# Kernel optimization log

Hardware: AMD Instinct MI355X
Metric: run time of the kernel (lower is better)

The kernel has to match this reference:

```python
import jax, jax.numpy as jnp
import numpy as np

CV_CHAN = 49  # displacement channels; radius = (CV_CHAN - 1) // 2 = 24


def conv1x1(x, W, b):
    # x: [B,C,H,Wd], W: [O,C], b: [O] -> [B,O,H,Wd]
    return jnp.einsum('oc,bchw->bohw', W, x) + b[None, :, None, None]


def corr_volume(f1, f2, radius, eps):
    """Shift-and-dot correlation along width. f1,f2: [B,C,H,W] -> [B,2r+1,H,W].
    Channel k corresponds to displacement d = k - radius; out-of-range positions are 0
    (handled by zero-padding, matching the torch zero-filled shifted tensors)."""
    f1n = f1 / (jnp.linalg.norm(f1, axis=1, keepdims=True) + eps)
    f2n = f2 / (jnp.linalg.norm(f2, axis=1, keepdims=True) + eps)
    Wd = f1.shape[3]
    pad = jnp.pad(f2n, ((0, 0), (0, 0), (0, 0), (radius, radius)))
    # shifted_k[x] = f2n[x - d] = pad[x + 2*radius - k]
    slices = [
        jnp.sum(f1n * jax.lax.dynamic_slice_in_dim(pad, 2 * radius - k, Wd, axis=3), axis=1)
        for k in range(2 * radius + 1)
    ]
    return jnp.stack(slices, axis=1)


def setup_inputs() -> dict:
    key = jax.random.key(0)
    ks = jax.random.split(key, 10)
    B, C, H, W = 4, 128, 128, 256
    F = 128  # fmap channels
    G = 96   # geo encoder output channels
    s = 0.05
    return {
        'feat_l1': jax.random.normal(ks[0], (B, C, H, W), jnp.float32),
        'feat_r1': jax.random.normal(ks[1], (B, C, H, W), jnp.float32),
        'cv0': jax.random.normal(ks[2], (B, CV_CHAN, H, W), jnp.float32),
        'cv1': jax.random.normal(ks[3], (B, CV_CHAN, H, W), jnp.float32),
        'cv2': jax.random.normal(ks[4], (B, CV_CHAN, H, W), jnp.float32),
        'W_f1': jax.random.normal(ks[5], (F, C), jnp.float32) * s,
        'b_f1': jnp.zeros((F,), jnp.float32),
        'W_f2': jax.random.normal(ks[6], (F, C), jnp.float32) * s,
        'b_f2': jnp.zeros((F,), jnp.float32),
        'W_geo': jax.random.normal(ks[7], (G, CV_CHAN), jnp.float32) * s,
        'b_geo': jnp.zeros((G,), jnp.float32),
        'W_sel': jax.random.normal(ks[8], (3, 3 * G), jnp.float32) * s,
        'b_sel': jnp.zeros((3,), jnp.float32),
    }


def reference(feat_l1, feat_r1, cv0, cv1, cv2,
              W_f1, b_f1, W_f2, b_f2, W_geo, b_geo, W_sel, b_sel):
    # init feature maps (init_fmap1 / init_fmap2 as 1x1 convs)
    fmap1 = conv1x1(feat_l1, W_f1, b_f1)
    fmap2 = conv1x1(feat_r1, W_f2, b_f2)
    radius = (CV_CHAN - 1) // 2
    init_corr = corr_volume(fmap1, fmap2, radius, 1e-8)  # [B, CV_CHAN, H, W]

    # geo_volume2 (1x1 conv CV_CHAN -> 96) applied to each geometric volume
    g0 = conv1x1(cv0, W_geo, b_geo)
    g1 = conv1x1(cv1, W_geo, b_geo)
    g2 = conv1x1(cv2, W_geo, b_geo)
    combined_g = jnp.concatenate([g0, g1, g2], axis=1)  # [B, 288, H, W]

    logits = conv1x1(combined_g, W_sel, b_sel)           # [B, 3, H, W]
    w = jax.nn.softmax(logits, axis=1)

    weighted = (w[:, 0:1] * cv0[:, :CV_CHAN]
                + w[:, 1:2] * cv1[:, :CV_CHAN]
                + w[:, 2:3] * cv2[:, :CV_CHAN])
    final = init_corr + weighted
    return (final, init_corr, w)
```

## Files before the change

kernel.cpp:

```cpp
#include <hip/hip_runtime.h>

#define HW 32768
#define WIDTH 256

typedef float f32x4 __attribute__((ext_vector_type(4)));
typedef short s16x8 __attribute__((ext_vector_type(8)));

__device__ __forceinline__ unsigned short f2bf(float f){
    unsigned int u = __float_as_uint(f);
    u += 0x7FFFu + ((u >> 16) & 1u);
    return (unsigned short)(u >> 16);
}
__device__ __forceinline__ unsigned int pk2(float a, float b){
    return (unsigned int)f2bf(a) | ((unsigned int)f2bf(b) << 16);
}

__global__ void k_wconv(const float* __restrict__ W1, const float* __restrict__ W2,
                        unsigned int* __restrict__ Wb)
{
    const int pi = blockIdx.x * 256 + threadIdx.x;
    const int j2   = pi & 3;
    const int l15  = (pi >> 2) & 15;
    const int quad = (pi >> 6) & 3;
    const int m    = (pi >> 8) & 7;
    const int kk   = (pi >> 11) & 3;
    const int F    = (pi >> 13) & 1;
    const float* Wm = F ? W2 : W1;
    const int row = m * 16 + l15;
    const int ch  = kk * 32 + quad * 8 + j2 * 2;
    Wb[pi] = pk2(Wm[row * 128 + ch], Wm[row * 128 + ch + 1]);
}

__global__ __launch_bounds__(256, 2) void k_fused(
    const float* __restrict__ fl, const float* __restrict__ fr,
    const unsigned int* __restrict__ Wbu,
    const float* __restrict__ b1, const float* __restrict__ b2,
    float* __restrict__ ic)
{
    __shared__ __align__(16) char pool[67584];
    __shared__ float s1[256], s2[256];
    unsigned short* f2s = (unsigned short*)pool;
    float* G            = (float*)pool;

    const int blk  = blockIdx.x;
    const int b    = blk >> 7;
    const int h    = blk & 127;
    const int tid  = threadIdx.x;
    const int wv   = tid >> 6;
    const int lane = tid & 63;
    const int quad = lane >> 4;
    const int l15  = lane & 15;

    const float* feats[2] = { fl + (size_t)b * 128 * HW + h * WIDTH,
                              fr + (size_t)b * 128 * HW + h * WIDTH };
    const float* bss[2]   = { b1, b2 };

    unsigned int f1p[64];

    #pragma unroll 1
    for (int Fi = 0; Fi < 2; ++Fi){
        const int F = 1 - Fi;
        const float* featB = feats[F];
        const float* bias  = bss[F];
        const unsigned int* WbF = Wbu + F * 8192;

        f32x4 acc[8][4];
        #pragma unroll
        for (int m = 0; m < 8; ++m)
            #pragma unroll
            for (int nt = 0; nt < 4; ++nt)
                acc[m][nt] = (f32x4){0.f, 0.f, 0.f, 0.f};

        float buf[3][8];
        #pragma unroll
        for (int t = 0; t < 2; ++t){
            const float* bp = featB + (size_t)(quad * 8) * HW + wv * 64 + t * 16 + l15;
            #pragma unroll
            for (int j = 0; j < 8; ++j) buf[t][j] = bp[(size_t)j * HW];
        }

        #pragma unroll
        for (int kk = 0; kk < 4; ++kk){
            s16x8 af[8];
            #pragma unroll
            for (int m = 0; m < 8; ++m)
                af[m] = *(const s16x8*)&WbF[(((kk * 8 + m) * 4 + quad) * 16 + l15) * 4];

            #pragma unroll
            for (int nt = 0; nt < 4; ++nt){
                const int t = kk * 4 + nt;
                if (t + 2 < 16){
                    const int kk2 = (t + 2) >> 2, nt2 = (t + 2) & 3;
                    const float* bp = featB + (size_t)(kk2 * 32 + quad * 8) * HW
                                      + wv * 64 + nt2 * 16 + l15;
                    #pragma unroll
                    for (int j = 0; j < 8; ++j) buf[(t + 2) % 3][j] = bp[(size_t)j * HW];
                }
                const float* cur = buf[t % 3];
                union { unsigned int u[4]; s16x8 v; } rb;
                rb.u[0] = pk2(cur[0], cur[1]); rb.u[1] = pk2(cur[2], cur[3]);
                rb.u[2] = pk2(cur[4], cur[5]); rb.u[3] = pk2(cur[6], cur[7]);
                #pragma unroll
                for (int m = 0; m < 8; ++m)
                    acc[m][nt] = __builtin_amdgcn_mfma_f32_16x16x32_bf16(af[m], rb.v, acc[m][nt], 0, 0, 0);
            }
        }

        float inv[4];
        #pragma unroll
        for (int nt = 0; nt < 4; ++nt){
            #pragma unroll
            for (int m = 0; m < 8; ++m)
                acc[m][nt] += *(const f32x4*)(bias + m * 16 + quad * 4);
            float n2 = 0.f;
            #pragma unroll
            for (int m = 0; m < 8; ++m)
                #pragma unroll
                for (int r = 0; r < 4; ++r)
                    n2 += acc[m][nt][r] * acc[m][nt][r];
            n2 += __shfl_xor(n2, 16, 64);
            n2 += __shfl_xor(n2, 32, 64);
            inv[nt] = 1.f / (sqrtf(n2) + 1e-8f);
        }

        if (F == 1){
            if (quad == 0){
                #pragma unroll
                for (int nt = 0; nt < 4; ++nt) s2[wv * 64 + nt * 16 + l15] = inv[nt];
            }
            #pragma unroll
            for (int nt = 0; nt < 4; ++nt){
                const int px = wv * 64 + nt * 16 + l15;
                #pragma unroll
                for (int m = 0; m < 8; ++m){
                    uint2 p;
                    p.x = pk2(acc[m][nt][0], acc[m][nt][1]);
                    p.y = pk2(acc[m][nt][2], acc[m][nt][3]);
                    *(uint2*)&f2s[px * 132 + m * 16 + quad * 4] = p;
                }
            }
        } else {
            #pragma unroll
            for (int m = 0; m < 8; ++m)
                #pragma unroll
                for (int nt = 0; nt < 4; ++nt){
                    f1p[m * 8 + nt * 2 + 0] = pk2(acc[m][nt][0], acc[m][nt][1]);
                    f1p[m * 8 + nt * 2 + 1] = pk2(acc[m][nt][2], acc[m][nt][3]);
                }
            if (quad == 0){
                #pragma unroll
                for (int nt = 0; nt < 4; ++nt) s1[wv * 64 + nt * 16 + l15] = inv[nt];
            }
        }
    }
    __syncthreads();

    f32x4 acc_c[4][4];
    #pragma unroll
    for (int st = 0; st < 4; ++st)
        #pragma unroll
        for (int ct = 0; ct < 4; ++ct)
            acc_c[st][ct] = (f32x4){0.f, 0.f, 0.f, 0.f};

    #pragma unroll
    for (int st = 0; st < 4; ++st){
        s16x8 afc[4];
        #pragma unroll
        for (int kk = 0; kk < 4; ++kk){
            union { unsigned int u[4]; s16x8 v; } r;
            #pragma unroll
            for (int j2 = 0; j2 < 4; ++j2){
                const int rp  = j2 & 1;
                const int qs  = (quad & 1) * 2 + (j2 >> 1);
                const int src = qs * 16 + l15;
                unsigned int a0 = (unsigned int)__shfl((int)f1p[(kk * 2 + 0) * 8 + st * 2 + rp], src, 64);
                unsigned int a1 = (unsigned int)__shfl((int)f1p[(kk * 2 + 1) * 8 + st * 2 + rp], src, 64);
                r.u[j2] = (quad >> 1) ? a1 : a0;
            }
            afc[kk] = r.v;
        }
        #pragma unroll
        for (int ct = 0; ct < 4; ++ct){
            const int s = wv * 64 + st * 16 + ct * 16 + l15 - 24;
            const bool valid = (s >= 0) && (s < WIDTH);
            const int sc = valid ? s : 0;
            #pragma unroll
            for (int kk = 0; kk < 4; ++kk){
                union { uint2 q2[2]; s16x8 v; } rb;
                rb.q2[0] = *(const uint2*)&f2s[sc * 132 + kk * 32 + quad * 8];
                rb.q2[1] = *(const uint2*)&f2s[sc * 132 + kk * 32 + quad * 8 + 4];
                s16x8 bf = rb.v;
                if (!valid) bf = (s16x8){0,0,0,0,0,0,0,0};
                acc_c[st][ct] = __builtin_amdgcn_mfma_f32_16x16x32_bf16(afc[kk], bf, acc_c[st][ct], 0, 0, 0);
            }
        }
    }
    __syncthreads();
    #pragma unroll
    for (int st = 0; st < 4; ++st)
        #pragma unroll
        for (int ct = 0; ct < 4; ++ct)
            #pragma unroll
            for (int r = 0; r < 4; ++r)
                G[((wv * 4 + st) * 16 + quad * 4 + r) * 66 + ct * 16 + l15] = acc_c[st][ct][r];
    __syncthreads();

    float* obase = ic + (size_t)b * 49 * HW + (size_t)h * WIDTH;
    #pragma unroll
    for (int st = 0; st < 4; ++st){
        const int gx = wv * 64 + st * 16;
        const float sc1 = s1[gx + l15];
        const float* Grow = &G[((wv * 4 + st) * 16 + l15) * 66];
        #pragma unroll
        for (int i = 0; i < 13; ++i){
            const int dd = quad + i * 4;
            if (dd < 49){
                int s2i = gx + l15 + 24 - dd;
                s2i = s2i < 0 ? 0 : (s2i > 255 ? 255 : s2i);
                const float v = Grow[l15 + 48 - dd] * sc1 * s2[s2i];
                obase[(size_t)dd * HW + gx + l15] = v;
            }
        }
    }
}

__global__ void k_prep(const float* __restrict__ Wsel, const float* __restrict__ bsel,
                       const float* __restrict__ Wgeo, const float* __restrict__ bgeo,
                       float* __restrict__ M, float* __restrict__ c0)
{
    int u = threadIdx.x;
    if (u < 441){
        int s = u / 147; int r = u % 147; int i = r / 49; int k = r % 49;
        float acc = 0.f;
        for (int o = 0; o < 96; ++o)
            acc += Wsel[s * 288 + i * 96 + o] * Wgeo[o * 49 + k];
        M[u] = acc;
    } else if (u < 444){
        int s = u - 441;
        float acc = bsel[s];
        for (int i = 0; i < 3; ++i)
            for (int o = 0; o < 96; ++o)
                acc += Wsel[s * 288 + i * 96 + o] * bgeo[o];
        c0[s] = acc;
    }
}

__global__ __launch_bounds__(256, 2) void k_sel(
    const float* __restrict__ cv0, const float* __restrict__ cv1, const float* __restrict__ cv2,
    const float* __restrict__ M, const float* __restrict__ c0,
    const float* __restrict__ ic,
    float* __restrict__ finalO, float* __restrict__ wO)
{
    __shared__ float Ms[441];
    __shared__ float c0s[3];
    const int tid = threadIdx.x;
    for (int i = tid; i < 441; i += 256) Ms[i] = M[i];
    if (tid < 3) c0s[tid] = c0[tid];
    __syncthreads();

    const int gid = blockIdx.x * 256 + tid;
    const int b = gid >> 15;
    const int p = gid & 32767;
    const size_t base = (size_t)b * 49 * HW + p;

    float a0[49], a1[49], a2[49];
    #pragma unroll
    for (int k = 0; k < 49; ++k){
        size_t o = base + (size_t)k * HW;
        a0[k] = cv0[o]; a1[k] = cv1[o]; a2[k] = cv2[o];
    }

    float lg0 = c0s[0], lg1 = c0s[1], lg2 = c0s[2];
    #pragma unroll
    for (int k = 0; k < 49; ++k){
        lg0 += Ms[k]       * a0[k] + Ms[49  + k] * a1[k] + Ms[98  + k] * a2[k];
        lg1 += Ms[147 + k] * a0[k] + Ms[196 + k] * a1[k] + Ms[245 + k] * a2[k];
        lg2 += Ms[294 + k] * a0[k] + Ms[343 + k] * a1[k] + Ms[392 + k] * a2[k];
    }
    float mx = fmaxf(lg0, fmaxf(lg1, lg2));
    float e0 = expf(lg0 - mx), e1 = expf(lg1 - mx), e2 = expf(lg2 - mx);
    float inv = 1.f / (e0 + e1 + e2);
    float w0 = e0 * inv, w1 = e1 * inv, w2 = e2 * inv;

    const size_t wbase = (size_t)b * 3 * HW + p;
    wO[wbase]          = w0;
    wO[wbase + HW]     = w1;
    wO[wbase + 2 * HW] = w2;

    #pragma unroll
    for (int k = 0; k < 49; ++k){
        size_t o = base + (size_t)k * HW;
        finalO[o] = ic[o] + w0 * a0[k] + w1 * a1[k] + w2 * a2[k];
    }
}

extern "C" void kernel_launch(void* const* d_in, const int* in_sizes, int n_in,
                              void* d_out, int out_size, void* d_ws, size_t ws_size,
                              hipStream_t stream)
{
    const float* feat_l1 = (const float*)d_in[0];
    const float* feat_r1 = (const float*)d_in[1];
    const float* cv0     = (const float*)d_in[2];
    const float* cv1     = (const float*)d_in[3];
    const float* cv2     = (const float*)d_in[4];
    const float* W_f1    = (const float*)d_in[5];
    const float* b_f1    = (const float*)d_in[6];
    const float* W_f2    = (const float*)d_in[7];
    const float* b_f2    = (const float*)d_in[8];
    const float* W_geo   = (const float*)d_in[9];
    const float* b_geo   = (const float*)d_in[10];
    const float* W_sel   = (const float*)d_in[11];
    const float* b_sel   = (const float*)d_in[12];

    float* finalO = (float*)d_out;
    float* icO    = (float*)d_out + 6422528;
    float* wO     = (float*)d_out + 12845056;

    unsigned int* Wb = (unsigned int*)d_ws;
    float* Mbuf  = (float*)((char*)d_ws + 65536);
    float* c0buf = Mbuf + 441;

    k_wconv<<<64, 256, 0, stream>>>(W_f1, W_f2, Wb);
    k_prep<<<1, 512, 0, stream>>>(W_sel, b_sel, W_geo, b_geo, Mbuf, c0buf);
    k_fused<<<512, 256, 0, stream>>>(feat_l1, feat_r1, Wb, b_f1, b_f2, icO);
    k_sel<<<512, 256, 0, stream>>>(cv0, cv1, cv2, Mbuf, c0buf, icO, finalO, wO);
}
```

Measured before the change: 274.8 us.

## Fuse selection softmax and final blend into correlation kernel epilogue

Folds the separate selection kernel into the correlation kernel's epilogue. Each thread handles one pixel of the row, computes the correlation values, reads the three cost volumes to form logits and softmax weights, then writes both init_corr and final. This removes the global re-read of init_corr and one kernel launch, and the two weight-prep kernels are merged into one. In exchange, each cost volume is read twice per pixel (the second read likely hits cache), the correlation is recomputed from shared memory, and the fused kernel carries more registers and LDS.

```diff
diff --git a/kernel.cpp b/kernel.cpp
--- a/kernel.cpp
+++ b/kernel.cpp
@@ -15,30 +15,57 @@
     return (unsigned int)f2bf(a) | ((unsigned int)f2bf(b) << 16);
 }
 
-__global__ void k_wconv(const float* __restrict__ W1, const float* __restrict__ W2,
-                        unsigned int* __restrict__ Wb)
+__global__ void k_pre(const float* __restrict__ W1, const float* __restrict__ W2,
+                      unsigned int* __restrict__ Wb,
+                      const float* __restrict__ Wsel, const float* __restrict__ bsel,
+                      const float* __restrict__ Wgeo, const float* __restrict__ bgeo,
+                      float* __restrict__ M, float* __restrict__ c0)
 {
-    const int pi = blockIdx.x * 256 + threadIdx.x;
-    const int j2   = pi & 3;
-    const int l15  = (pi >> 2) & 15;
-    const int quad = (pi >> 6) & 3;
-    const int m    = (pi >> 8) & 7;
-    const int kk   = (pi >> 11) & 3;
-    const int F    = (pi >> 13) & 1;
-    const float* Wm = F ? W2 : W1;
-    const int row = m * 16 + l15;
-    const int ch  = kk * 32 + quad * 8 + j2 * 2;
-    Wb[pi] = pk2(Wm[row * 128 + ch], Wm[row * 128 + ch + 1]);
+    if (blockIdx.x < 64){
+        const int pi = blockIdx.x * 256 + threadIdx.x;
+        const int j2   = pi & 3;
+        const int l15  = (pi >> 2) & 15;
+        const int quad = (pi >> 6) & 3;
+        const int m    = (pi >> 8) & 7;
+        const int kk   = (pi >> 11) & 3;
+        const int F    = (pi >> 13) & 1;
+        const float* Wm = F ? W2 : W1;
+        const int row = m * 16 + l15;
+        const int ch  = kk * 32 + quad * 8 + j2 * 2;
+        Wb[pi] = pk2(Wm[row * 128 + ch], Wm[row * 128 + ch + 1]);
+    } else {
+        for (int u = threadIdx.x; u < 444; u += 256){
+            if (u < 441){
+                int s = u / 147; int r = u % 147; int i = r / 49; int k = r % 49;
+                float acc = 0.f;
+                for (int o = 0; o < 96; ++o)
+                    acc += Wsel[s * 288 + i * 96 + o] * Wgeo[o * 49 + k];
+                M[u] = acc;
+            } else {
+                int s = u - 441;
+                float acc = bsel[s];
+                for (int i = 0; i < 3; ++i)
+                    for (int o = 0; o < 96; ++o)
+                        acc += Wsel[s * 288 + i * 96 + o] * bgeo[o];
+                c0[s] = acc;
+            }
+        }
+    }
 }
 
 __global__ __launch_bounds__(256, 2) void k_fused(
     const float* __restrict__ fl, const float* __restrict__ fr,
     const unsigned int* __restrict__ Wbu,
     const float* __restrict__ b1, const float* __restrict__ b2,
-    float* __restrict__ ic)
+    const float* __restrict__ cv0, const float* __restrict__ cv1,
+    const float* __restrict__ cv2,
+    const float* __restrict__ Mg, const float* __restrict__ c0g,
+    float* __restrict__ icO, float* __restrict__ finalO, float* __restrict__ wO)
 {
     __shared__ __align__(16) char pool[67584];
     __shared__ float s1[256], s2[256];
+    __shared__ float Ms[441];
+    __shared__ float c0s[3];
     unsigned short* f2s = (unsigned short*)pool;
     float* G            = (float*)pool;
 
@@ -50,6 +77,9 @@
     const int lane = tid & 63;
     const int quad = lane >> 4;
     const int l15  = lane & 15;
+
+    for (int i = tid; i < 441; i += 256) Ms[i] = Mg[i];
+    if (tid < 3) c0s[tid] = c0g[tid];
 
     const float* feats[2] = { fl + (size_t)b * 128 * HW + h * WIDTH,
                               fr + (size_t)b * 128 * HW + h * WIDTH };
@@ -205,92 +235,50 @@
                 G[((wv * 4 + st) * 16 + quad * 4 + r) * 66 + ct * 16 + l15] = acc_c[st][ct][r];
     __syncthreads();
 
-    float* obase = ic + (size_t)b * 49 * HW + (size_t)h * WIDTH;
-    #pragma unroll
-    for (int st = 0; st < 4; ++st){
-        const int gx = wv * 64 + st * 16;
-        const float sc1 = s1[gx + l15];
-        const float* Grow = &G[((wv * 4 + st) * 16 + l15) * 66];
-        #pragma unroll
-        for (int i = 0; i < 13; ++i){
-            const int dd = quad + i * 4;
-            if (dd < 49){
-                int s2i = gx + l15 + 24 - dd;
-                s2i = s2i < 0 ? 0 : (s2i > 255 ? 255 : s2i);
-                const float v = Grow[l15 + 48 - dd] * sc1 * s2[s2i];
-                obase[(size_t)dd * HW + gx + l15] = v;
-            }
-        }
-    }
-}
-
-__global__ void k_prep(const float* __restrict__ Wsel, const float* __restrict__ bsel,
-                       const float* __restrict__ Wgeo, const float* __restrict__ bgeo,
-                       float* __restrict__ M, float* __restrict__ c0)
-{
-    int u = threadIdx.x;
-    if (u < 441){
-        int s = u / 147; int r = u % 147; int i = r / 49; int k = r % 49;
-        float acc = 0.f;
-        for (int o = 0; o < 96; ++o)
-            acc += Wsel[s * 288 + i * 96 + o] * Wgeo[o * 49 + k];
-        M[u] = acc;
-    } else if (u < 444){
-        int s = u - 441;
-        float acc = bsel[s];
-        for (int i = 0; i < 3; ++i)
-            for (int o = 0; o < 96; ++o)
-                acc += Wsel[s * 288 + i * 96 + o] * bgeo[o];
-        c0[s] = acc;
-    }
-}
-
-__global__ __launch_bounds__(256, 2) void k_sel(
-    const float* __restrict__ cv0, const float* __restrict__ cv1, const float* __restrict__ cv2,
-    const float* __restrict__ M, const float* __restrict__ c0,
-    const float* __restrict__ ic,
-    float* __restrict__ finalO, float* __restrict__ wO)
-{
-    __shared__ float Ms[441];
-    __shared__ float c0s[3];
-    const int tid = threadIdx.x;
-    for (int i = tid; i < 441; i += 256) Ms[i] = M[i];
-    if (tid < 3) c0s[tid] = c0[tid];
-    __syncthreads();
-
-    const int gid = blockIdx.x * 256 + tid;
-    const int b = gid >> 15;
-    const int p = gid & 32767;
-    const size_t base = (size_t)b * 49 * HW + p;
-
-    float a0[49], a1[49], a2[49];
-    #pragma unroll
-    for (int k = 0; k < 49; ++k){
-        size_t o = base + (size_t)k * HW;
-        a0[k] = cv0[o]; a1[k] = cv1[o]; a2[k] = cv2[o];
-    }
+    const int px = tid;
+    const float sc1 = s1[px];
+    const float* Gp = &G[px * 66 + (px & 15) + 48];
+    const size_t rowoff = (size_t)h * WIDTH + px;
+    const size_t cvbase = (size_t)b * 49 * HW + rowoff;
+    float* icb = icO    + cvbase;
+    float* fnb = finalO + cvbase;
+    const float* c0p = cv0 + cvbase;
+    const float* c1p = cv1 + cvbase;
+    const float* c2p = cv2 + cvbase;
 
     float lg0 = c0s[0], lg1 = c0s[1], lg2 = c0s[2];
-    #pragma unroll
-    for (int k = 0; k < 49; ++k){
-        lg0 += Ms[k]       * a0[k] + Ms[49  + k] * a1[k] + Ms[98  + k] * a2[k];
-        lg1 += Ms[147 + k] * a0[k] + Ms[196 + k] * a1[k] + Ms[245 + k] * a2[k];
-        lg2 += Ms[294 + k] * a0[k] + Ms[343 + k] * a1[k] + Ms[392 + k] * a2[k];
-    }
-    float mx = fmaxf(lg0, fmaxf(lg1, lg2));
-    float e0 = expf(lg0 - mx), e1 = expf(lg1 - mx), e2 = expf(lg2 - mx);
-    float inv = 1.f / (e0 + e1 + e2);
-    float w0 = e0 * inv, w1 = e1 * inv, w2 = e2 * inv;
-
-    const size_t wbase = (size_t)b * 3 * HW + p;
-    wO[wbase]          = w0;
-    wO[wbase + HW]     = w1;
-    wO[wbase + 2 * HW] = w2;
-
-    #pragma unroll
-    for (int k = 0; k < 49; ++k){
-        size_t o = base + (size_t)k * HW;
-        finalO[o] = ic[o] + w0 * a0[k] + w1 * a1[k] + w2 * a2[k];
+    #pragma unroll 7
+    for (int dd = 0; dd < 49; ++dd){
+        int s2i = px + 24 - dd;
+        s2i = s2i < 0 ? 0 : (s2i > 255 ? 255 : s2i);
+        const float icv = Gp[-dd] * sc1 * s2[s2i];
+        icb[(size_t)dd * HW] = icv;
+        const float a0 = c0p[(size_t)dd * HW];
+        const float a1 = c1p[(size_t)dd * HW];
+        const float a2 = c2p[(size_t)dd * HW];
+        lg0 += Ms[dd]       * a0 + Ms[49  + dd] * a1 + Ms[98  + dd] * a2;
+        lg1 += Ms[147 + dd] * a0 + Ms[196 + dd] * a1 + Ms[245 + dd] * a2;
+        lg2 += Ms[294 + dd] * a0 + Ms[343 + dd] * a1 + Ms[392 + dd] * a2;
+    }
+
+    const float mx = fmaxf(lg0, fmaxf(lg1, lg2));
+    const float e0 = expf(lg0 - mx), e1 = expf(lg1 - mx), e2 = expf(lg2 - mx);
+    const float einv = 1.f / (e0 + e1 + e2);
+    const float w0 = e0 * einv, w1 = e1 * einv, w2 = e2 * einv;
+
+    float* wb = wO + (size_t)b * 3 * HW + rowoff;
+    wb[0]      = w0;
+    wb[HW]     = w1;
+    wb[2 * HW] = w2;
+
+    #pragma unroll 7
+    for (int dd = 0; dd < 49; ++dd){
+        int s2i = px + 24 - dd;
+        s2i = s2i < 0 ? 0 : (s2i > 255 ? 255 : s2i);
+        const float icv = Gp[-dd] * sc1 * s2[s2i];
+        fnb[(size_t)dd * HW] = icv + w0 * c0p[(size_t)dd * HW]
+                                   + w1 * c1p[(size_t)dd * HW]
+                                   + w2 * c2p[(size_t)dd * HW];
     }
 }
 
@@ -320,8 +308,8 @@
     float* Mbuf  = (float*)((char*)d_ws + 65536);
     float* c0buf = Mbuf + 441;
 
-    k_wconv<<<64, 256, 0, stream>>>(W_f1, W_f2, Wb);
-    k_prep<<<1, 512, 0, stream>>>(W_sel, b_sel, W_geo, b_geo, Mbuf, c0buf);
-    k_fused<<<512, 256, 0, stream>>>(feat_l1, feat_r1, Wb, b_f1, b_f2, icO);
-    k_sel<<<512, 256, 0, stream>>>(cv0, cv1, cv2, Mbuf, c0buf, icO, finalO, wO);
-}
+    k_pre<<<65, 256, 0, stream>>>(W_f1, W_f2, Wb, W_sel, b_sel, W_geo, b_geo, Mbuf, c0buf);
+    k_fused<<<512, 256, 0, stream>>>(feat_l1, feat_r1, Wb, b_f1, b_f2,
+                                     cv0, cv1, cv2, Mbuf, c0buf,
+                                     icO, finalO, wO);
+}
```

Result: no change. 274.9 us (+0.0%).
